# Optimization experiments

Hardware: AMD Instinct MI355X
Metric: run time of the kernel (lower is better)

## Reference

```python
import jax, jax.numpy as jnp
import numpy as np

P = 16
PW = P // 2 + 1  # 9, rfft width


def setup_inputs() -> dict:
    key = jax.random.key(0)
    ks = jax.random.split(key, 5)
    B, C, H, W = 128, 3, 224, 224
    E = 768
    N = (H // P) * (W // P)  # 196
    return {
        "x": jax.random.normal(ks[0], (B, C, H, W), dtype=jnp.float32),
        "freq_weight_h": jnp.ones((P,), dtype=jnp.float32),
        "freq_weight_w": jnp.ones((PW,), dtype=jnp.float32),
        "proj_w": jax.random.normal(ks[1], (E, C * P * PW), dtype=jnp.float32) * 0.02,
        "proj_b": jnp.zeros((E,), dtype=jnp.float32),
        "cls_token": jax.random.normal(ks[2], (1, 1, E), dtype=jnp.float32),
        "pos_emb": jax.random.normal(ks[3], (1, N + 1, E), dtype=jnp.float32),
    }


def reference(x, freq_weight_h, freq_weight_w, proj_w, proj_b, cls_token, pos_emb):
    B, C, H, W = x.shape
    nH, nW = H // P, W // P
    N = nH * nW
    # unfold into non-overlapping PxP patches: (B, C, N, P, P)
    patches = x.reshape(B, C, nH, P, nW, P).transpose(0, 1, 2, 4, 3, 5)
    patches = patches.reshape(B, C, N, P, P)
    # rfft2 with ortho norm, keep real part: (B, C, N, P, PW)
    x_fft = jnp.fft.rfft2(patches, norm="ortho").real
    # frequency reweighting
    x_fft = x_fft * freq_weight_h[None, None, None, :, None]
    x_fft = x_fft * freq_weight_w[None, None, None, None, :]
    # (B, N, C*P*PW)
    x_flat = x_fft.transpose(0, 2, 1, 3, 4).reshape(B, N, C * P * PW)
    # linear projection to embed_dim
    x_proj = jnp.einsum("bnf,ef->bne", x_flat, proj_w) + proj_b
    # prepend cls token, add position embeddings (dropout is eval/identity)
    cls = jnp.broadcast_to(cls_token, (B, 1, cls_token.shape[-1]))
    out = jnp.concatenate([cls, x_proj], axis=1) + pos_emb
    return out
```

## Files before the change

kernel.cpp:

```cpp
#include <hip/hip_runtime.h>
#include <hip/hip_bf16.h>

typedef __bf16 bf16;
typedef __attribute__((ext_vector_type(8))) __bf16 bf16x8;
typedef __attribute__((ext_vector_type(4))) float floatx4;

#define PP 16
#define PPW 9
#define CFEAT 432
#define EDIM 768
#define KDIM 768
#define NPAT 196
#define NBATCH 128
#define MROWS (NBATCH * NPAT)

#define NB_W 2304
#define NB_CLS 384
#define NB_UNF 9408
#define NB_PREP (NB_W + NB_CLS + NB_UNF)

__device__ inline void gload16(const void* g, void* l) {
  __builtin_amdgcn_global_load_lds(
      (const __attribute__((address_space(1))) void*)g,
      (__attribute__((address_space(3))) void*)l, 16, 0, 0);
}

__global__ __launch_bounds__(256) void prep_kernel(
    const float* __restrict__ x, const float* __restrict__ pw,
    const float* __restrict__ fwh, const float* __restrict__ fww,
    const float* __restrict__ cls, const float* __restrict__ pos,
    bf16* __restrict__ Wb, bf16* __restrict__ A, float* __restrict__ out) {
  const int blk = blockIdx.x;
  const int t = threadIdx.x;

  if (blk >= NB_W + NB_CLS) {
    const int i = (blk - NB_W - NB_CLS) * 256 + t;
    const int w8 = i % 28;
    const int tmp = i / 28;
    const int h = tmp % 224;
    const int tmp2 = tmp / 224;
    const int c = tmp2 % 3;
    const int b = tmp2 / 3;
    const float4 f0 = *reinterpret_cast<const float4*>(x + (size_t)i * 8);
    const float4 f1 = *reinterpret_cast<const float4*>(x + (size_t)i * 8 + 4);
    bf16x8 v;
    v[0] = (bf16)f0.x; v[1] = (bf16)f0.y; v[2] = (bf16)f0.z; v[3] = (bf16)f0.w;
    v[4] = (bf16)f1.x; v[5] = (bf16)f1.y; v[6] = (bf16)f1.z; v[7] = (bf16)f1.w;
    const int row = b * NPAT + (h >> 4) * 14 + (w8 >> 1);
    const int k = c * 256 + (h & 15) * 16 + (w8 & 1) * 8;
    *reinterpret_cast<bf16x8*>(A + (size_t)row * KDIM + k) = v;
  } else if (blk < NB_W) {
    __shared__ float s_pw[144];
    __shared__ float s_fh[16];
    __shared__ float s_fw[9];
    __shared__ float s_cos[16];
    const int e = blk / 3;
    const int c = blk % 3;
    if (t < 144) s_pw[t] = pw[e * CFEAT + c * 144 + t];
    if (t < 16) {
      s_fh[t] = fwh[t];
      s_cos[t] = cosf((float)t * 0.39269908169872414f);
    }
    if (t < 9) s_fw[t] = fww[t];
    __syncthreads();
    const int h = t >> 4, w = t & 15;
    float acc = 0.f;
#pragma unroll
    for (int u = 0; u < 16; ++u) {
      const float fh = s_fh[u];
      const int uh = (u * h) & 15;
#pragma unroll
      for (int v = 0; v < 9; ++v) {
        acc += s_pw[u * 9 + v] * s_fw[v] * s_cos[(uh + v * w) & 15] * fh;
      }
    }
    Wb[e * KDIM + c * 256 + t] = (bf16)(acc * 0.0625f);
  } else {
    const int idx = (blk - NB_W) * 256 + t;
    const int b = idx / 768;
    const int e = idx - b * 768;
    out[(size_t)b * 197 * 768 + e] = cls[e] + pos[e];
  }
}

__global__ __launch_bounds__(256) void gemm_db_kernel(
    const bf16* __restrict__ A, const bf16* __restrict__ Wb,
    const float* __restrict__ pb, const float* __restrict__ pos,
    float* __restrict__ out) {
  __shared__ __align__(16) bf16 sA[2][128 * 32];
  __shared__ __align__(16) bf16 sB[2][128 * 32];

  const int bid = blockIdx.x;
  const int swz = (bid & 7) * 147 + (bid >> 3);
  const int mt = swz / 6;
  const int nt = swz - mt * 6;
  const int t = threadIdx.x;
  const int l = t & 63;
  const int wv = t >> 6;
  const int wm = wv >> 1, wn = wv & 1;

  const bf16* gA = A + ((size_t)(mt * 128) + (t >> 2)) * KDIM + (t & 3) * 8;
  const bf16* gB = Wb + ((size_t)(nt * 128) + (t >> 2)) * KDIM + (t & 3) * 8;
  const size_t rstep = (size_t)64 * KDIM;
  const int lbase = wv * 512;

#define STAGE(buf, ko)                                  \
  do {                                                  \
    gload16(gA + (ko), &sA[buf][lbase]);                \
    gload16(gA + rstep + (ko), &sA[buf][2048 + lbase]); \
    gload16(gB + (ko), &sB[buf][lbase]);                \
    gload16(gB + rstep + (ko), &sB[buf][2048 + lbase]); \
  } while (0)

  floatx4 acc[4][4];
#pragma unroll
  for (int i = 0; i < 4; ++i)
#pragma unroll
    for (int j = 0; j < 4; ++j) acc[i][j] = (floatx4){0.f, 0.f, 0.f, 0.f};

  const int lr = l & 15;
  const int lk = (l >> 4) * 8;

#define COMPUTE(buf)                                              \
  do {                                                            \
    bf16x8 af[4], bfr[4];                                         \
    _Pragma("unroll") for (int mi = 0; mi < 4; ++mi) af[mi] =     \
        *reinterpret_cast<const bf16x8*>(                         \
            &sA[buf][(wm * 64 + mi * 16 + lr) * 32 + lk]);        \
    _Pragma("unroll") for (int ni = 0; ni < 4; ++ni) bfr[ni] =    \
        *reinterpret_cast<const bf16x8*>(                         \
            &sB[buf][(wn * 64 + ni * 16 + lr) * 32 + lk]);        \
    _Pragma("unroll") for (int mi = 0; mi < 4; ++mi)              \
        _Pragma("unroll") for (int ni = 0; ni < 4; ++ni) acc[mi]  \
            [ni] = __builtin_amdgcn_mfma_f32_16x16x32_bf16(       \
                af[mi], bfr[ni], acc[mi][ni], 0, 0, 0);           \
  } while (0)

  STAGE(0, 0);
  __syncthreads();
  int cur = 0;
  for (int kt = 0; kt < 23; ++kt) {
    STAGE(cur ^ 1, (kt + 1) * 32);
    COMPUTE(cur);
    __syncthreads();
    cur ^= 1;
  }
  COMPUTE(cur);
#undef STAGE
#undef COMPUTE

  float pbv[4];
#pragma unroll
  for (int ni = 0; ni < 4; ++ni)
    pbv[ni] = pb[nt * 128 + wn * 64 + ni * 16 + (l & 15)];

#pragma unroll
  for (int mi = 0; mi < 4; ++mi) {
#pragma unroll
    for (int j = 0; j < 4; ++j) {
      const unsigned m = wm * 64 + mi * 16 + ((l >> 4) << 2) + j;
      const unsigned Rr = mt * 128u + m;
      const unsigned b2 = Rr / 196u;
      const unsigned np2 = Rr - b2 * 196u;
      float* orow = out + ((size_t)b2 * 197 + 1 + np2) * 768;
      const float* prow = pos + (size_t)(1 + np2) * 768;
#pragma unroll
      for (int ni = 0; ni < 4; ++ni) {
        const int e = nt * 128 + wn * 64 + ni * 16 + (l & 15);
        orow[e] = acc[mi][ni][j] + pbv[ni] + prow[e];
      }
    }
  }
}

extern "C" void kernel_launch(void* const* d_in, const int* in_sizes, int n_in,
                              void* d_out, int out_size, void* d_ws,
                              size_t ws_size, hipStream_t stream) {
  const float* x = (const float*)d_in[0];
  const float* fwh = (const float*)d_in[1];
  const float* fww = (const float*)d_in[2];
  const float* proj_w = (const float*)d_in[3];
  const float* proj_b = (const float*)d_in[4];
  const float* cls = (const float*)d_in[5];
  const float* pos = (const float*)d_in[6];
  float* out = (float*)d_out;

  const size_t needW = (size_t)EDIM * KDIM * sizeof(bf16);
  bf16* Wb = (bf16*)d_ws;
  bf16* A = (bf16*)((char*)d_ws + needW);

  prep_kernel<<<NB_PREP, 256, 0, stream>>>(x, proj_w, fwh, fww, cls, pos, Wb,
                                           A, out);
  gemm_db_kernel<<<1176, 256, 0, stream>>>(A, Wb, proj_b, pos, out);
}
```

Baseline: 77.80 us.

## Restructure GEMM into 256x128 tiles with 8-wave phased pipeline and swizzled LDS

Replaces the 128x128 double-buffered GEMM with a 512-thread, 256x128 tile kernel. It uses a four-slot LDS pipeline in which global-to-LDS loads for future K-steps are issued between the fragment reads and the MFMAs, and waits use vmcnt instead of a full drain. LDS rows are XOR-swizzled to avoid bank conflicts, MFMA sections run at raised wave priority, and the block-to-XCD mapping is remapped for 588 blocks. This aims to hide load latency and raise B-tile reuse, at the cost of more LDS per block and lower occupancy.

```diff
diff --git a/kernel.cpp b/kernel.cpp
--- a/kernel.cpp
+++ b/kernel.cpp
@@ -83,33 +83,45 @@
   }
 }
 
-__global__ __launch_bounds__(256) void gemm_db_kernel(
+__global__ __launch_bounds__(512) void gemm_8ph_kernel(
     const bf16* __restrict__ A, const bf16* __restrict__ Wb,
     const float* __restrict__ pb, const float* __restrict__ pos,
     float* __restrict__ out) {
-  __shared__ __align__(16) bf16 sA[2][128 * 32];
-  __shared__ __align__(16) bf16 sB[2][128 * 32];
+  __shared__ __align__(16) bf16 sA[2 * 2 * 8192];
+  __shared__ __align__(16) bf16 sB[2 * 2 * 4096];
 
   const int bid = blockIdx.x;
-  const int swz = (bid & 7) * 147 + (bid >> 3);
-  const int mt = swz / 6;
-  const int nt = swz - mt * 6;
+  const int xcd = bid & 7;
+  const int idx = bid >> 3;
+  const int wgid = (xcd < 4 ? xcd * 74 : 296 + (xcd - 4) * 73) + idx;
+  const int mt = wgid / 6;
+  const int nt = wgid - mt * 6;
+
   const int t = threadIdx.x;
   const int l = t & 63;
   const int wv = t >> 6;
-  const int wm = wv >> 1, wn = wv & 1;
-
-  const bf16* gA = A + ((size_t)(mt * 128) + (t >> 2)) * KDIM + (t & 3) * 8;
-  const bf16* gB = Wb + ((size_t)(nt * 128) + (t >> 2)) * KDIM + (t & 3) * 8;
-  const size_t rstep = (size_t)64 * KDIM;
-  const int lbase = wv * 512;
-
-#define STAGE(buf, ko)                                  \
-  do {                                                  \
-    gload16(gA + (ko), &sA[buf][lbase]);                \
-    gload16(gA + rstep + (ko), &sA[buf][2048 + lbase]); \
-    gload16(gB + (ko), &sB[buf][lbase]);                \
-    gload16(gB + rstep + (ko), &sB[buf][2048 + lbase]); \
+  const int wm = wv >> 1;
+  const int wn = wv & 1;
+  const int lr = l & 15, lq = l >> 4;
+
+  const int ra0 = t >> 2, ra1 = (512 + t) >> 2;
+  const int qa0 = (t & 3) ^ ((ra0 ^ (ra0 >> 2)) & 3);
+  const int qa1 = (t & 3) ^ ((ra1 ^ (ra1 >> 2)) & 3);
+  const bf16* gA0 = A + (size_t)(mt * 256 + ra0) * KDIM + qa0 * 8;
+  const bf16* gA1 = A + (size_t)(mt * 256 + ra1) * KDIM + qa1 * 8;
+  const int rb0 = t >> 2;
+  const int qb0 = (t & 3) ^ ((rb0 ^ (rb0 >> 2)) & 3);
+  const bf16* gB0 = Wb + (size_t)(nt * 128 + rb0) * KDIM + qb0 * 8;
+
+#define SLOTA(b, s) (sA + ((b)*2 + (s)) * 8192)
+#define SLOTB(b, s) (sB + ((b)*2 + (s)) * 4096)
+
+#define STAGE(b, s, kts)                                   \
+  do {                                                     \
+    const int ko = (kts)*64 + (s)*32;                      \
+    gload16(gA0 + ko, SLOTA(b, s) + wv * 512);             \
+    gload16(gA1 + ko, SLOTA(b, s) + 4096 + wv * 512);      \
+    gload16(gB0 + ko, SLOTB(b, s) + wv * 512);             \
   } while (0)
 
   floatx4 acc[4][4];
@@ -118,55 +130,77 @@
 #pragma unroll
     for (int j = 0; j < 4; ++j) acc[i][j] = (floatx4){0.f, 0.f, 0.f, 0.f};
 
-  const int lr = l & 15;
-  const int lk = (l >> 4) * 8;
-
-#define COMPUTE(buf)                                              \
-  do {                                                            \
-    bf16x8 af[4], bfr[4];                                         \
-    _Pragma("unroll") for (int mi = 0; mi < 4; ++mi) af[mi] =     \
-        *reinterpret_cast<const bf16x8*>(                         \
-            &sA[buf][(wm * 64 + mi * 16 + lr) * 32 + lk]);        \
-    _Pragma("unroll") for (int ni = 0; ni < 4; ++ni) bfr[ni] =    \
-        *reinterpret_cast<const bf16x8*>(                         \
-            &sB[buf][(wn * 64 + ni * 16 + lr) * 32 + lk]);        \
-    _Pragma("unroll") for (int mi = 0; mi < 4; ++mi)              \
-        _Pragma("unroll") for (int ni = 0; ni < 4; ++ni) acc[mi]  \
-            [ni] = __builtin_amdgcn_mfma_f32_16x16x32_bf16(       \
-                af[mi], bfr[ni], acc[mi][ni], 0, 0, 0);           \
+#define PHASE(b, s, sb, ss, skt)                                        \
+  do {                                                                  \
+    bf16x8 af[4], bfr[4];                                               \
+    _Pragma("unroll") for (int mf = 0; mf < 4; ++mf) {                  \
+      const int r = wm * 64 + mf * 16 + lr;                             \
+      const int qp = lq ^ ((r ^ (r >> 2)) & 3);                         \
+      af[mf] = *reinterpret_cast<const bf16x8*>(SLOTA(b, s) + r * 32 +  \
+                                                qp * 8);                \
+    }                                                                   \
+    _Pragma("unroll") for (int nf = 0; nf < 4; ++nf) {                  \
+      const int r = wn * 64 + nf * 16 + lr;                             \
+      const int qp = lq ^ ((r ^ (r >> 2)) & 3);                         \
+      bfr[nf] = *reinterpret_cast<const bf16x8*>(SLOTB(b, s) + r * 32 + \
+                                                 qp * 8);               \
+    }                                                                   \
+    STAGE(sb, ss, skt);                                                 \
+    asm volatile("" ::: "memory");                                      \
+    __builtin_amdgcn_s_barrier();                                       \
+    __builtin_amdgcn_s_setprio(1);                                      \
+    _Pragma("unroll") for (int mf = 0; mf < 4; ++mf)                    \
+        _Pragma("unroll") for (int nf = 0; nf < 4; ++nf) acc[mf][nf] =  \
+            __builtin_amdgcn_mfma_f32_16x16x32_bf16(af[mf], bfr[nf],    \
+                                                    acc[mf][nf], 0, 0,  \
+                                                    0);                 \
+    __builtin_amdgcn_s_setprio(0);                                      \
+    asm volatile("s_waitcnt vmcnt(6)" ::: "memory");                    \
+    __builtin_amdgcn_s_barrier();                                       \
   } while (0)
 
-  STAGE(0, 0);
-  __syncthreads();
-  int cur = 0;
-  for (int kt = 0; kt < 23; ++kt) {
-    STAGE(cur ^ 1, (kt + 1) * 32);
-    COMPUTE(cur);
-    __syncthreads();
-    cur ^= 1;
+  STAGE(0, 0, 0);
+  STAGE(0, 1, 0);
+  STAGE(1, 0, 1);
+  asm volatile("s_waitcnt vmcnt(6)" ::: "memory");
+  __builtin_amdgcn_s_barrier();
+
+#define TILE(B, KT)                                  \
+  do {                                               \
+    const int k1 = (KT) + 1 < 12 ? (KT) + 1 : 11;    \
+    const int k2 = (KT) + 2 < 12 ? (KT) + 2 : 11;    \
+    PHASE(B, 0, (B) ^ 1, 1, k1);                     \
+    PHASE(B, 1, (B), 0, k2);                         \
+  } while (0)
+
+  for (int kt2 = 0; kt2 < 12; kt2 += 2) {
+    TILE(0, kt2);
+    TILE(1, kt2 + 1);
   }
-  COMPUTE(cur);
+#undef TILE
+#undef PHASE
 #undef STAGE
-#undef COMPUTE
+#undef SLOTA
+#undef SLOTB
 
   float pbv[4];
 #pragma unroll
   for (int ni = 0; ni < 4; ++ni)
-    pbv[ni] = pb[nt * 128 + wn * 64 + ni * 16 + (l & 15)];
+    pbv[ni] = pb[nt * 128 + wn * 64 + ni * 16 + lr];
 
 #pragma unroll
   for (int mi = 0; mi < 4; ++mi) {
 #pragma unroll
     for (int j = 0; j < 4; ++j) {
-      const unsigned m = wm * 64 + mi * 16 + ((l >> 4) << 2) + j;
-      const unsigned Rr = mt * 128u + m;
+      const unsigned m = wm * 64 + mi * 16 + lq * 4 + j;
+      const unsigned Rr = mt * 256u + m;
       const unsigned b2 = Rr / 196u;
       const unsigned np2 = Rr - b2 * 196u;
       float* orow = out + ((size_t)b2 * 197 + 1 + np2) * 768;
       const float* prow = pos + (size_t)(1 + np2) * 768;
 #pragma unroll
       for (int ni = 0; ni < 4; ++ni) {
-        const int e = nt * 128 + wn * 64 + ni * 16 + (l & 15);
+        const int e = nt * 128 + wn * 64 + ni * 16 + lr;
         orow[e] = acc[mi][ni][j] + pbv[ni] + prow[e];
       }
     }
@@ -191,5 +225,5 @@
 
   prep_kernel<<<NB_PREP, 256, 0, stream>>>(x, proj_w, fwh, fww, cls, pos, Wb,
                                            A, out);
-  gemm_db_kernel<<<1176, 256, 0, stream>>>(A, Wb, proj_b, pos, out);
-}
+  gemm_8ph_kernel<<<588, 512, 0, stream>>>(A, Wb, proj_b, pos, out);
+}
```

Result: slower. 87.04 us (+11.9%).

## Replace LDS-staged GEMM with direct global-to-register double-buffered fragment loads

Applied to the files above, without the earlier changes.

The GEMM kernel drops shared-memory staging and barriers. Each wave loads its MFMA fragments straight from global memory into a two-deep register double buffer, with the k-loop fully unrolled. This removes LDS writes and reads and the __syncthreads cost. In exchange, waves that share tiles load the same data redundantly, and each load covers only 64 contiguous bytes per row.

```diff
diff --git a/kernel.cpp b/kernel.cpp
--- a/kernel.cpp
+++ b/kernel.cpp
@@ -18,12 +18,6 @@
 #define NB_CLS 384
 #define NB_UNF 9408
 #define NB_PREP (NB_W + NB_CLS + NB_UNF)
-
-__device__ inline void gload16(const void* g, void* l) {
-  __builtin_amdgcn_global_load_lds(
-      (const __attribute__((address_space(1))) void*)g,
-      (__attribute__((address_space(3))) void*)l, 16, 0, 0);
-}
 
 __global__ __launch_bounds__(256) void prep_kernel(
     const float* __restrict__ x, const float* __restrict__ pw,
@@ -83,13 +77,10 @@
   }
 }
 
-__global__ __launch_bounds__(256) void gemm_db_kernel(
+__global__ __launch_bounds__(256) void gemm_nolds_kernel(
     const bf16* __restrict__ A, const bf16* __restrict__ Wb,
     const float* __restrict__ pb, const float* __restrict__ pos,
     float* __restrict__ out) {
-  __shared__ __align__(16) bf16 sA[2][128 * 32];
-  __shared__ __align__(16) bf16 sB[2][128 * 32];
-
   const int bid = blockIdx.x;
   const int swz = (bid & 7) * 147 + (bid >> 3);
   const int mt = swz / 6;
@@ -98,19 +89,18 @@
   const int l = t & 63;
   const int wv = t >> 6;
   const int wm = wv >> 1, wn = wv & 1;
+  const int lr = l & 15, lq = l >> 4;
 
-  const bf16* gA = A + ((size_t)(mt * 128) + (t >> 2)) * KDIM + (t & 3) * 8;
-  const bf16* gB = Wb + ((size_t)(nt * 128) + (t >> 2)) * KDIM + (t & 3) * 8;
-  const size_t rstep = (size_t)64 * KDIM;
-  const int lbase = wv * 512;
-
-#define STAGE(buf, ko)                                  \
-  do {                                                  \
-    gload16(gA + (ko), &sA[buf][lbase]);                \
-    gload16(gA + rstep + (ko), &sA[buf][2048 + lbase]); \
-    gload16(gB + (ko), &sB[buf][lbase]);                \
-    gload16(gB + rstep + (ko), &sB[buf][2048 + lbase]); \
-  } while (0)
+  const bf16* baseA[4];
+  const bf16* baseB[4];
+#pragma unroll
+  for (int mi = 0; mi < 4; ++mi)
+    baseA[mi] =
+        A + (size_t)(mt * 128 + wm * 64 + mi * 16 + lr) * KDIM + lq * 8;
+#pragma unroll
+  for (int ni = 0; ni < 4; ++ni)
+    baseB[ni] =
+        Wb + (size_t)(nt * 128 + wn * 64 + ni * 16 + lr) * KDIM + lq * 8;
 
   floatx4 acc[4][4];
 #pragma unroll
@@ -118,47 +108,49 @@
 #pragma unroll
     for (int j = 0; j < 4; ++j) acc[i][j] = (floatx4){0.f, 0.f, 0.f, 0.f};
 
-  const int lr = l & 15;
-  const int lk = (l >> 4) * 8;
+  bf16x8 abuf[2][4], bbuf[2][4];
 
-#define COMPUTE(buf)                                              \
-  do {                                                            \
-    bf16x8 af[4], bfr[4];                                         \
-    _Pragma("unroll") for (int mi = 0; mi < 4; ++mi) af[mi] =     \
-        *reinterpret_cast<const bf16x8*>(                         \
-            &sA[buf][(wm * 64 + mi * 16 + lr) * 32 + lk]);        \
-    _Pragma("unroll") for (int ni = 0; ni < 4; ++ni) bfr[ni] =    \
-        *reinterpret_cast<const bf16x8*>(                         \
-            &sB[buf][(wn * 64 + ni * 16 + lr) * 32 + lk]);        \
-    _Pragma("unroll") for (int mi = 0; mi < 4; ++mi)              \
-        _Pragma("unroll") for (int ni = 0; ni < 4; ++ni) acc[mi]  \
-            [ni] = __builtin_amdgcn_mfma_f32_16x16x32_bf16(       \
-                af[mi], bfr[ni], acc[mi][ni], 0, 0, 0);           \
+#define LOADF(P, kt)                                                        \
+  do {                                                                      \
+    _Pragma("unroll") for (int mi = 0; mi < 4; ++mi) abuf[P][mi] =          \
+        *reinterpret_cast<const bf16x8*>(baseA[mi] + (kt)*32);              \
+    _Pragma("unroll") for (int ni = 0; ni < 4; ++ni) bbuf[P][ni] =          \
+        *reinterpret_cast<const bf16x8*>(baseB[ni] + (kt)*32);              \
   } while (0)
 
-  STAGE(0, 0);
-  __syncthreads();
-  int cur = 0;
-  for (int kt = 0; kt < 23; ++kt) {
-    STAGE(cur ^ 1, (kt + 1) * 32);
-    COMPUTE(cur);
-    __syncthreads();
-    cur ^= 1;
+#define MMF(P)                                                             \
+  do {                                                                     \
+    _Pragma("unroll") for (int mi = 0; mi < 4; ++mi)                       \
+        _Pragma("unroll") for (int ni = 0; ni < 4; ++ni) acc[mi][ni] =     \
+            __builtin_amdgcn_mfma_f32_16x16x32_bf16(abuf[P][mi],           \
+                                                    bbuf[P][ni],           \
+                                                    acc[mi][ni], 0, 0, 0); \
+  } while (0)
+
+  LOADF(0, 0);
+  LOADF(1, 1);
+#pragma unroll
+  for (int it = 0; it < 11; ++it) {
+    MMF(0);
+    LOADF(0, 2 * it + 2);
+    MMF(1);
+    LOADF(1, 2 * it + 3);
   }
-  COMPUTE(cur);
-#undef STAGE
-#undef COMPUTE
+  MMF(0);
+  MMF(1);
+#undef LOADF
+#undef MMF
 
   float pbv[4];
 #pragma unroll
   for (int ni = 0; ni < 4; ++ni)
-    pbv[ni] = pb[nt * 128 + wn * 64 + ni * 16 + (l & 15)];
+    pbv[ni] = pb[nt * 128 + wn * 64 + ni * 16 + lr];
 
 #pragma unroll
   for (int mi = 0; mi < 4; ++mi) {
 #pragma unroll
     for (int j = 0; j < 4; ++j) {
-      const unsigned m = wm * 64 + mi * 16 + ((l >> 4) << 2) + j;
+      const unsigned m = wm * 64 + mi * 16 + lq * 4 + j;
       const unsigned Rr = mt * 128u + m;
       const unsigned b2 = Rr / 196u;
       const unsigned np2 = Rr - b2 * 196u;
@@ -166,7 +158,7 @@
       const float* prow = pos + (size_t)(1 + np2) * 768;
 #pragma unroll
       for (int ni = 0; ni < 4; ++ni) {
-        const int e = nt * 128 + wn * 64 + ni * 16 + (l & 15);
+        const int e = nt * 128 + wn * 64 + ni * 16 + lr;
         orow[e] = acc[mi][ni][j] + pbv[ni] + prow[e];
       }
     }
@@ -191,5 +183,5 @@
 
   prep_kernel<<<NB_PREP, 256, 0, stream>>>(x, proj_w, fwh, fww, cls, pos, Wb,
                                            A, out);
-  gemm_db_kernel<<<1176, 256, 0, stream>>>(A, Wb, proj_b, pos, out);
+  gemm_nolds_kernel<<<1176, 256, 0, stream>>>(A, Wb, proj_b, pos, out);
 }
```

Result: slower. 147.3 us (+89.3%).
